# Optimization experiments

Hardware: AMD Instinct MI355X
Metric: run time of the kernel (lower is better)

The kernel has to match this reference:

```python
import jax, jax.numpy as jnp
import numpy as np

# Config from module init / global Args
H = 8        # n_head
DK = 64      # d_k
DV = 64      # d_v
D = 512      # d_model
KSZ = 3      # kernel_size (args.kernel_size)
B_PARAM = 0.001
CUR_HEAD = 3
ALPHA_C = -float(np.log(B_PARAM / (H - 1) * CUR_HEAD))  # alpha_c (nonzero head)
EPS = 1e-6


def setup_inputs() -> dict:
    key = jax.random.key(0)
    ks = jax.random.split(key, 8)
    B, L = 2, 2048
    q = jax.random.normal(ks[0], (B, L, D), jnp.float32)
    k = jax.random.normal(ks[1], (B, L, D), jnp.float32)
    v = jax.random.normal(ks[2], (B, L, D), jnp.float32)
    # Linear weights stored torch-style: [out_features, in_features]
    w_q = jax.random.normal(ks[3], (H * DK, D), jnp.float32) * 0.02
    w_k = jax.random.normal(ks[4], (H * DK, D), jnp.float32) * 0.02
    w_v = jax.random.normal(ks[5], (H * DV, D), jnp.float32) * 0.02
    w_fc = jax.random.normal(ks[6], (D, H * DV), jnp.float32) * 0.02
    gamma = jnp.ones((D,), jnp.float32)
    beta = jnp.zeros((D,), jnp.float32)
    return {"q": q, "k": k, "v": v, "w_q": w_q, "w_k": w_k, "w_v": w_v,
            "w_fc": w_fc, "gamma": gamma, "beta": beta}


def reference(q, k, v, w_q, w_k, w_v, w_fc, gamma, beta):
    B, L, _ = q.shape
    residual = q
    # QKV projections -> [B, H, L, d]
    qh = jnp.einsum('bld,ed->ble', q, w_q).reshape(B, L, H, DK).transpose(0, 2, 1, 3)
    kh = jnp.einsum('bld,ed->ble', k, w_k).reshape(B, L, H, DK).transpose(0, 2, 1, 3)
    vh = jnp.einsum('bld,ed->ble', v, w_v).reshape(B, L, H, DV).transpose(0, 2, 1, 3)
    # Scores: matmul(q / sqrt(d_k), k^T)  (LaSAttention receives d_k = d_k**0.5)
    attn = jnp.einsum('bhqd,bhkd->bhqk', qh, kh) / jnp.sqrt(jnp.float32(DK))
    # Distance weighting: eld = alpha_c * -(x - y) * attn, d_l[i,j] = j - i
    idx = jnp.arange(L)
    d_l = idx[None, :] - idx[:, None]                      # [L, L]
    eld_mat = (-ALPHA_C * d_l).astype(attn.dtype)
    eld = eld_mat[None, None, :, :] * attn
    # Softmax then avg_pool1d(kernel=KSZ, stride=1, pad=(KSZ-1)//2, count_include_pad)
    p = jax.nn.softmax(eld, axis=-1)                       # [B, H, L, L]
    pad = (KSZ - 1) // 2
    pp = jnp.pad(p, ((0, 0), (0, 0), (0, 0), (pad, pad)))
    pooled = sum(pp[..., j:j + L] for j in range(KSZ)) / jnp.float32(KSZ)
    # Value matmul (seq lengths equal so no trimming needed)
    out = jnp.einsum('bhqk,bhkd->bhqd', pooled, vh)
    out = out.transpose(0, 2, 1, 3).reshape(B, L, H * DV)
    # Output projection (dropout is identity in eval), residual, LayerNorm
    out = jnp.einsum('ble,de->bld', out, w_fc)
    out = out[:, :, None, :] + residual[:, :, None, :]     # [B, L, 1, D]
    mu = out.mean(axis=-1, keepdims=True)
    var = ((out - mu) ** 2).mean(axis=-1, keepdims=True)
    out = (out - mu) / jnp.sqrt(var + EPS) * gamma + beta
    return (out, pooled)
```

## Files before the change

kernel.cpp:

```cpp
#include <hip/hip_runtime.h>
#include <cstddef>
#include <cstdint>

#define ALPHA_C 7.7550531393693407f
constexpr int BB = 2;
constexpr int LL = 2048;
constexpr int HH = 8;
constexpr size_t OUT0  = (size_t)BB * LL * 512;
constexpr size_t PLANE = (size_t)BB * HH * LL * 64;
constexpr size_t XN    = (size_t)BB * LL * 512;
constexpr size_t WN    = (size_t)512 * 512;

typedef __attribute__((ext_vector_type(8))) short bf16x8;
typedef __attribute__((ext_vector_type(4))) short short4v;
typedef __attribute__((ext_vector_type(4))) float f32x4;

__device__ inline short f2bf(float x) {
  union { float f; unsigned u; } un; un.f = x;
  unsigned r = un.u + 0x7fffu + ((un.u >> 16) & 1u);
  return (short)(r >> 16);
}
__device__ inline float bf2f(short s) {
  union { unsigned u; float f; } un; un.u = ((unsigned)(unsigned short)s) << 16;
  return un.f;
}
__device__ inline void split3(float x, short& h, short& m, short& l) {
  h = f2bf(x); float r = x - bf2f(h);
  m = f2bf(r); float r2 = r - bf2f(m);
  l = f2bf(r2);
}

__global__ __launch_bounds__(256) void k_split3x(
    const float* __restrict__ a, const float* __restrict__ b, const float* __restrict__ c,
    short* __restrict__ da, short* __restrict__ db, short* __restrict__ dc, size_t n)
{
  size_t i = ((size_t)blockIdx.x * 256 + threadIdx.x) * 4;
  if (i >= n) return;
  const float* srcs[3] = {a, b, c};
  short* dsts[3] = {da, db, dc};
  #pragma unroll
  for (int s = 0; s < 3; ++s) {
    float4 x = *(const float4*)&srcs[s][i];
    short4v h, m, l;
    short th, tm, tl;
// ... 104 lines not shown
    for (int t = 0; t < 4; ++t) {
      const int e = n0 + t * 16 + colg, h = e >> 6, dk = e & 63;
      #pragma unroll
      for (int r = 0; r < 4; ++r) {
        const int m = m0 + w * 16 + quad * 4 + r;
        const int b = m >> 11, l = m & 2047;
        size_t base = ((size_t)(b * HH + h) * LL + l) * 64 + dk;
        short hh, mm, ll; split3(acc[t][r], hh, mm, ll);
        Y[base] = hh; Y[PLANE + base] = mm; Y[2 * PLANE + base] = ll;
      }
    }
  } else {
    const int b  = m0 >> 11;
    const int l0 = (m0 & 2047) + w * 16 + quad * 4;
    #pragma unroll
    for (int t = 0; t < 4; ++t) {
      const int e = n0 + t * 16 + colg, h = e >> 6, dk = e & 63;
      short4v s;
      #pragma unroll
      for (int r = 0; r < 4; ++r) s[r] = f2bf(acc[t][r]);
      *(short4v*)&vt[(((size_t)b * HH + h) * 64 + dk) * LL + l0] = s;
    }
  }
}

__global__ __launch_bounds__(256) void k_stats(
    const short* __restrict__ qs, const short* __restrict__ ks,
    float* __restrict__ statspart)
{
  const int i0 = blockIdx.x * 64;
  const int jh = blockIdx.y;
  const int bh = blockIdx.z;
  __shared__ short Ks[3][64 * 72];
  const int tid = threadIdx.x;
  const int lane = tid & 63, w = tid >> 6;
  const int quad = lane >> 4, colg = lane & 15, l15 = lane & 15;
  const int sr8 = tid >> 3, sc8 = (tid & 7) * 8;

  bf16x8 qf[3][2];
  {
    const size_t qoff = ((size_t)bh * LL + i0 + w * 16 + l15) * 64 + (quad << 3);
    #pragma unroll
    for (int p = 0; p < 3; ++p)
      #pragma unroll
      for (int ch = 0; ch < 2; ++ch)
        qf[p][ch] = *(const bf16x8*)&qs[p * PLANE + qoff + ch * 32];
  }

  const int jt0 = jh * 16;
  const short* kbase = ks + (size_t)bh * LL * 64;
  #pragma unroll
  for (int p = 0; p < 3; ++p)
    #pragma unroll
    for (int it = 0; it < 2; ++it) {
      int r = it * 32 + sr8;
      *(bf16x8*)&Ks[p][r * 72 + sc8] =
          *(const bf16x8*)&kbase[p * PLANE + ((size_t)jt0 * 64 + r) * 64 + sc8];
    }
  __syncthreads();

  float M[4], S[4];
  #pragma unroll
  for (int r = 0; r < 4; ++r) { M[r] = -3.0e38f; S[r] = 0.f; }

  for (int jj = 0; jj < 16; ++jj) {
    const int jt = jt0 + jj;
    const int j0 = jt * 64;
    bf16x8 kreg[3][2];
    if (jj + 1 < 16) {
      #pragma unroll
      for (int p = 0; p < 3; ++p)
        #pragma unroll
        for (int it = 0; it < 2; ++it) {
          int r = it * 32 + sr8;
          kreg[p][it] = *(const bf16x8*)&kbase[p * PLANE + ((size_t)(jt + 1) * 64 + r) * 64 + sc8];
        }
    }

    f32x4 acc[4];
    #pragma unroll
    for (int t = 0; t < 4; ++t) { acc[t][0]=0.f; acc[t][1]=0.f; acc[t][2]=0.f; acc[t][3]=0.f; }
    #pragma unroll
    for (int ch = 0; ch < 2; ++ch) {
      const int ka = (quad << 3) + ch * 32;
      #pragma unroll
      for (int t = 0; t < 4; ++t) {
        const int br = (t * 16 + l15) * 72 + ka;
        bf16x8 bh_ = *(const bf16x8*)&Ks[0][br];
        bf16x8 bm_ = *(const bf16x8*)&Ks[1][br];
        bf16x8 bl_ = *(const bf16x8*)&Ks[2][br];
        acc[t] = __builtin_amdgcn_mfma_f32_16x16x32_bf16(qf[0][ch], bh_, acc[t], 0, 0, 0);
        acc[t] = __builtin_amdgcn_mfma_f32_16x16x32_bf16(qf[0][ch], bm_, acc[t], 0, 0, 0);
        acc[t] = __builtin_amdgcn_mfma_f32_16x16x32_bf16(qf[1][ch], bh_, acc[t], 0, 0, 0);
        acc[t] = __builtin_amdgcn_mfma_f32_16x16x32_bf16(qf[0][ch], bl_, acc[t], 0, 0, 0);
        acc[t] = __builtin_amdgcn_mfma_f32_16x16x32_bf16(qf[2][ch], bh_, acc[t], 0, 0, 0);
        acc[t] = __builtin_amdgcn_mfma_f32_16x16x32_bf16(qf[1][ch], bm_, acc[t], 0, 0, 0);
      }
    }

    #pragma unroll
    for (int r = 0; r < 4; ++r) {
      const int irow = i0 + w * 16 + quad * 4 + r;
      float e0 = -ALPHA_C * (float)(j0 +  0 + colg - irow) * (acc[0][r] * 0.125f);
      float e1 = -ALPHA_C * (float)(j0 + 16 + colg - irow) * (acc[1][r] * 0.125f);
      float e2 = -ALPHA_C * (float)(j0 + 32 + colg - irow) * (acc[2][r] * 0.125f);
      float e3 = -ALPHA_C * (float)(j0 + 48 + colg - irow) * (acc[3][r] * 0.125f);
      float mx = fmaxf(fmaxf(e0, e1), fmaxf(e2, e3));
      float nM = fmaxf(M[r], mx);
      S[r] = S[r] * __expf(M[r] - nM)
           + __expf(e0 - nM) + __expf(e1 - nM) + __expf(e2 - nM) + __expf(e3 - nM);
      M[r] = nM;
    }

    __syncthreads();
    if (jj + 1 < 16) {
      #pragma unroll
      for (int p = 0; p < 3; ++p)
        #pragma unroll
        for (int it = 0; it < 2; ++it) {
          int r = it * 32 + sr8;
          *(bf16x8*)&Ks[p][r * 72 + sc8] = kreg[p][it];
        }
    }
    __syncthreads();
  }

  #pragma unroll
  for (int r = 0; r < 4; ++r) {
    float M_ = M[r], S_ = S[r];
    #pragma unroll
    for (int d = 1; d < 16; d <<= 1) {
      float Mo = __shfl_xor(M_, d);
      float So = __shfl_xor(S_, d);
      float nM = fmaxf(M_, Mo);
      S_ = S_ * __expf(M_ - nM) + So * __expf(Mo - nM);
      M_ = nM;
    }
    if (colg == 0) {
      int irow = i0 + w * 16 + quad * 4 + r;
      size_t idx = (((size_t)jh * 16 + bh) * LL + irow) * 2;
      statspart[idx] = M_; statspart[idx + 1] = S_;
    }
  }
}

__global__ __launch_bounds__(256) void k_mergestats(
    const float* __restrict__ statspart, float* __restrict__ rowstats)
{
  const size_t row = (size_t)blockIdx.x * 256 + threadIdx.x;
  float2 a = *(const float2*)&statspart[row * 2];
  float2 b = *(const float2*)&statspart[(size_t)16 * LL * 2 + row * 2];
  float nM = fmaxf(a.x, b.x);
  float S = a.y * __expf(a.x - nM) + b.y * __expf(b.x - nM);
  rowstats[row * 2] = nM; rowstats[row * 2 + 1] = S;
}

__global__ __launch_bounds__(256) void k_pool_pv(
    const short* __restrict__ qs, const short* __restrict__ ks,
    const short* __restrict__ vavgt, const float* __restrict__ rowstats,
    float* __restrict__ pooled, short* __restrict__ outh)
{
  const int i0 = blockIdx.x * 64;
  const int bh = blockIdx.y;
  const int b = bh >> 3, h = bh & 7;
  float*       Pg = pooled + (size_t)bh * LL * LL;
  const short* Vt = vavgt + (size_t)bh * 64 * LL;
  const short* kbase = ks + (size_t)bh * LL * 64;

  __shared__ short Ks[3][64 * 72];
  __shared__ short Vsm[64 * 72];
  __shared__ short Pa[2][64 * 72];
  __shared__ float Mrow[64], invSr[64], lhalo[64];

  const int tid = threadIdx.x;
  const int lane = tid & 63, w = tid >> 6;
  const int quad = lane >> 4, colg = lane & 15, l15 = lane & 15;
  const int sr8 = tid >> 3, sc8 = (tid & 7) * 8;

  bf16x8 qf[3][2];
  {
    const size_t qoff = ((size_t)bh * LL + i0 + w * 16 + l15) * 64 + (quad << 3);
    #pragma unroll
    for (int p = 0; p < 3; ++p)
      #pragma unroll
      for (int ch = 0; ch < 2; ++ch)
        qf[p][ch] = *(const bf16x8*)&qs[p * PLANE + qoff + ch * 32];
  }
  if (tid < 64) {
    float2 ms = *(const float2*)&rowstats[((size_t)bh * LL + i0 + tid) * 2];
    Mrow[tid] = ms.x; invSr[tid] = 1.0f / ms.y; lhalo[tid] = 0.f;
  }

  #pragma unroll
  for (int p = 0; p < 3; ++p)
    #pragma unroll
    for (int it = 0; it < 2; ++it) {
      int r = it * 32 + sr8;
      *(bf16x8*)&Ks[p][r * 72 + sc8] = *(const bf16x8*)&kbase[p * PLANE + (size_t)r * 64 + sc8];
    }
  __syncthreads();

  f32x4 pv[4];
  #pragma unroll
  for (int t = 0; t < 4; ++t) { pv[t][0]=0.f; pv[t][1]=0.f; pv[t][2]=0.f; pv[t][3]=0.f; }

  for (int jt = 0; jt <= 32; ++jt) {
    if (jt < 32) {
      const int j0 = jt * 64;
      f32x4 acc[4];
      #pragma unroll
      for (int t = 0; t < 4; ++t) { acc[t][0]=0.f; acc[t][1]=0.f; acc[t][2]=0.f; acc[t][3]=0.f; }
      #pragma unroll
      for (int ch = 0; ch < 2; ++ch) {
        const int ka = (quad << 3) + ch * 32;
        #pragma unroll
        for (int t = 0; t < 4; ++t) {
          const int br = (t * 16 + l15) * 72 + ka;
          bf16x8 bh_ = *(const bf16x8*)&Ks[0][br];
          bf16x8 bm_ = *(const bf16x8*)&Ks[1][br];
          bf16x8 bl_ = *(const bf16x8*)&Ks[2][br];
          acc[t] = __builtin_amdgcn_mfma_f32_16x16x32_bf16(qf[0][ch], bh_, acc[t], 0, 0, 0);
          acc[t] = __builtin_amdgcn_mfma_f32_16x16x32_bf16(qf[0][ch], bm_, acc[t], 0, 0, 0);
          acc[t] = __builtin_amdgcn_mfma_f32_16x16x32_bf16(qf[1][ch], bh_, acc[t], 0, 0, 0);
          acc[t] = __builtin_amdgcn_mfma_f32_16x16x32_bf16(qf[0][ch], bl_, acc[t], 0, 0, 0);
          acc[t] = __builtin_amdgcn_mfma_f32_16x16x32_bf16(qf[2][ch], bh_, acc[t], 0, 0, 0);
          acc[t] = __builtin_amdgcn_mfma_f32_16x16x32_bf16(qf[1][ch], bm_, acc[t], 0, 0, 0);
        }
      }
      short* Pc = Pa[jt & 1];
      #pragma unroll
      for (int r = 0; r < 4; ++r) {
        const int row = w * 16 + quad * 4 + r;
        const int irow = i0 + row;
        const float Mr = Mrow[row], iS = invSr[row];
        #pragma unroll
        for (int t = 0; t < 4; ++t) {
          int jl = t * 16 + colg;
          float e = -ALPHA_C * (float)(j0 + jl - irow) * (acc[t][r] * 0.125f);
          Pc[row * 72 + jl] = f2bf(__expf(e - Mr) * iS);
        }
      }
    }
    if (jt >= 1) {
      #pragma unroll
      for (int it = 0; it < 2; ++it) {
        int d = it * 32 + sr8;
        *(bf16x8*)&Vsm[d * 72 + sc8] = *(const bf16x8*)&Vt[(size_t)d * LL + (jt - 1) * 64 + sc8];
      }
    }
    __syncthreads();

    if (jt >= 1) {
      const short* Pp = Pa[(jt - 1) & 1];
      const short* Pn = Pa[jt & 1];
      #pragma unroll
      for (int u = 0; u < 2; ++u) {
        const int row = (u == 0) ? (tid >> 3) : (tid >> 3) + 32;
        const int c0 = (tid & 7) * 8;
        bf16x8 x = *(const bf16x8*)&Pp[row * 72 + c0];
        float xf[8];
        #pragma unroll
        for (int i = 0; i < 8; ++i) xf[i] = bf2f(x[i]);
        float lft = (c0 == 0)  ? lhalo[row] : bf2f(Pp[row * 72 + c0 - 1]);
        float rgt = (c0 == 56) ? ((jt < 32) ? bf2f(Pn[row * 72]) : 0.f)
                               : bf2f(Pp[row * 72 + c0 + 8]);
        f32x4 o0, o1;
        o0[0] = (lft   + xf[0] + xf[1]) * (1.0f/3.0f);
        o0[1] = (xf[0] + xf[1] + xf[2]) * (1.0f/3.0f);
        o0[2] = (xf[1] + xf[2] + xf[3]) * (1.0f/3.0f);
        o0[3] = (xf[2] + xf[3] + xf[4]) * (1.0f/3.0f);
        o1[0] = (xf[3] + xf[4] + xf[5]) * (1.0f/3.0f);
        o1[1] = (xf[4] + xf[5] + xf[6]) * (1.0f/3.0f);
        o1[2] = (xf[5] + xf[6] + xf[7]) * (1.0f/3.0f);
        o1[3] = (xf[6] + xf[7] + rgt  ) * (1.0f/3.0f);
        float* dst = &Pg[(size_t)(i0 + row) * LL + (jt - 1) * 64 + c0];
        __builtin_nontemporal_store(o0, (f32x4*)dst);
        __builtin_nontemporal_store(o1, (f32x4*)(dst + 4));
        if (c0 == 56) lhalo[row] = xf[7];
      }
      #pragma unroll
      for (int ch = 0; ch < 2; ++ch) {
        const int ka = (quad << 3) + ch * 32;
        bf16x8 af = *(const bf16x8*)&Pp[(w * 16 + l15) * 72 + ka];
        #pragma unroll
        for (int t = 0; t < 4; ++t) {
          bf16x8 bfv = *(const bf16x8*)&Vsm[(t * 16 + l15) * 72 + ka];
          pv[t] = __builtin_amdgcn_mfma_f32_16x16x32_bf16(af, bfv, pv[t], 0, 0, 0);
        }
      }
    }
    if (jt + 1 < 32) {
      #pragma unroll
      for (int p = 0; p < 3; ++p)
        #pragma unroll
        for (int it = 0; it < 2; ++it) {
          int r = it * 32 + sr8;
          *(bf16x8*)&Ks[p][r * 72 + sc8] =
              *(const bf16x8*)&kbase[p * PLANE + ((size_t)(jt + 1) * 64 + r) * 64 + sc8];
        }
    }
    __syncthreads();
  }

  #pragma unroll
  for (int t = 0; t < 4; ++t)
    #pragma unroll
    for (int r = 0; r < 4; ++r) {
      int i = i0 + w * 16 + quad * 4 + r;
      int d = t * 16 + colg;
      outh[((size_t)b * LL + i) * 512 + h * 64 + d] = f2bf(pv[t][r]);
    }
}

__global__ __launch_bounds__(256) void k_fc(
    const short* __restrict__ outh, const short* __restrict__ wfcb, float* __restrict__ fcout)
{
  const int n0 = blockIdx.x * 64;
  const int m0 = blockIdx.y * 64;
  __shared__ short Asm[64 * 72];
  __shared__ short Bsm[64 * 72];
  const int tid = threadIdx.x;
  const int lane = tid & 63, w = tid >> 6;
  const int sr8 = tid >> 3, sc8 = (tid & 7) * 8;

  f32x4 acc[4];
  #pragma unroll
  for (int t = 0; t < 4; ++t) { acc[t][0]=0.f; acc[t][1]=0.f; acc[t][2]=0.f; acc[t][3]=0.f; }

  for (int k0 = 0; k0 < 512; k0 += 64) {
    #pragma unroll
    for (int it = 0; it < 2; ++it) {
      int r = it * 32 + sr8;
      *(bf16x8*)&Asm[r * 72 + sc8] = *(const bf16x8*)&outh[(size_t)(m0 + r) * 512 + k0 + sc8];
      *(bf16x8*)&Bsm[r * 72 + sc8] = *(const bf16x8*)&wfcb[(size_t)(n0 + r) * 512 + k0 + sc8];
    }
    __syncthreads();
    #pragma unroll
    for (int ch = 0; ch < 2; ++ch) {
      const int ka = ((lane >> 4) << 3) + ch * 32;
      bf16x8 af = *(const bf16x8*)&Asm[(w * 16 + (lane & 15)) * 72 + ka];
      #pragma unroll
      for (int t = 0; t < 4; ++t) {
        bf16x8 bfv = *(const bf16x8*)&Bsm[(t * 16 + (lane & 15)) * 72 + ka];
        acc[t] = __builtin_amdgcn_mfma_f32_16x16x32_bf16(af, bfv, acc[t], 0, 0, 0);
// ... 44 lines not shown
}

extern "C" void kernel_launch(void* const* d_in, const int* in_sizes, int n_in,
                              void* d_out, int out_size, void* d_ws, size_t ws_size,
                              hipStream_t stream)
{
  const float* q     = (const float*)d_in[0];
  const float* k     = (const float*)d_in[1];
  const float* v     = (const float*)d_in[2];
  const float* wq    = (const float*)d_in[3];
  const float* wk    = (const float*)d_in[4];
  const float* wv    = (const float*)d_in[5];
  const float* wfc   = (const float*)d_in[6];
  const float* gamma = (const float*)d_in[7];
  const float* beta  = (const float*)d_in[8];

  float* out    = (float*)d_out;
  float* pooled = out + OUT0;

  short* xq    = (short*)d_ws;
  short* xk    = xq + 3 * XN;
  short* xv    = xk + 3 * XN;
  short* wq3   = xv + 3 * XN;
  short* wk3   = wq3 + 3 * WN;
  short* wv3   = wk3 + 3 * WN;
  short* qsp   = wv3 + 3 * WN;
  short* ksp   = qsp + 3 * PLANE;
  short* vt    = ksp + 3 * PLANE;
  short* vavgt = vt + PLANE;
  short* wfcb  = vavgt + PLANE;
  short* outh  = wfcb + WN;
  float* statspart = (float*)(outh + OUT0);
  float* rowstats  = statspart + 4 * (size_t)BB * HH * LL;
  float* fcout     = rowstats + 2 * (size_t)BB * HH * LL;

  k_split3x<<<dim3((unsigned)(XN / 4 / 256)), 256, 0, stream>>>(q, k, v, xq, xk, xv, XN);
  k_split3x<<<dim3((unsigned)(WN / 4 / 256)), 256, 0, stream>>>(wq, wk, wv, wq3, wk3, wv3, WN);
  k_cvtbf  <<<dim3((unsigned)(WN / 8 / 256)), 256, 0, stream>>>(wfc, wfcb, WN);
  k_proj   <<<dim3(24, 64), 256, 0, stream>>>(xq, xk, xv, wq3, wk3, wv3, qsp, ksp, vt);
  k_vavg   <<<dim3(1024),   256, 0, stream>>>(vt, vavgt);
  k_stats  <<<dim3(32, 2, 16), 256, 0, stream>>>(qsp, ksp, statspart);
  k_mergestats<<<dim3(128), 256, 0, stream>>>(statspart, rowstats);
  k_pool_pv<<<dim3(32, 16), 256, 0, stream>>>(qsp, ksp, vavgt, rowstats, pooled, outh);
  k_fc     <<<dim3(8, 64),  256, 0, stream>>>(outh, wfcb, fcout);
  k_ln     <<<dim3(4096),   256, 0, stream>>>(fcout, q, gamma, beta, out);
}
```

Baseline: 496.7 us.

## Tile QK score MFMAs as 2x2 warp grid to halve LDS K reads

In both the stats and pool/PV kernels, each warp now computes a 32x32 sub-tile (two row groups by two column groups) instead of a 16x64 strip. Each K fragment read from shared memory is then reused across two row groups, which halves LDS traffic for the score computation at the cost of more Q fragment registers. The stats kernel merges the two column-half partial max/sum pairs through shared memory. The pool kernel folds the softmax normalization into a single per-row log-sum constant held in registers, exp(e - (M + log S)), replacing the shared-memory max and reciprocal-sum lookup and the multiply.

```diff
diff --git a/kernel.cpp b/kernel.cpp
--- a/kernel.cpp
+++ b/kernel.cpp
@@ -180,19 +180,22 @@
   const int jh = blockIdx.y;
   const int bh = blockIdx.z;
   __shared__ short Ks[3][64 * 72];
+  __shared__ float2 MSsm[2][64];
   const int tid = threadIdx.x;
   const int lane = tid & 63, w = tid >> 6;
+  const int wr = w >> 1, wc = w & 1;
   const int quad = lane >> 4, colg = lane & 15, l15 = lane & 15;
   const int sr8 = tid >> 3, sc8 = (tid & 7) * 8;
 
-  bf16x8 qf[3][2];
-  {
-    const size_t qoff = ((size_t)bh * LL + i0 + w * 16 + l15) * 64 + (quad << 3);
+  bf16x8 qf[2][3][2];
+  #pragma unroll
+  for (int rg = 0; rg < 2; ++rg) {
+    const size_t qoff = ((size_t)bh * LL + i0 + wr * 32 + rg * 16 + l15) * 64 + (quad << 3);
     #pragma unroll
     for (int p = 0; p < 3; ++p)
       #pragma unroll
       for (int ch = 0; ch < 2; ++ch)
-        qf[p][ch] = *(const bf16x8*)&qs[p * PLANE + qoff + ch * 32];
+        qf[rg][p][ch] = *(const bf16x8*)&qs[p * PLANE + qoff + ch * 32];
   }
 
   const int jt0 = jh * 16;
@@ -207,9 +210,11 @@
     }
   __syncthreads();
 
-  float M[4], S[4];
-  #pragma unroll
-  for (int r = 0; r < 4; ++r) { M[r] = -3.0e38f; S[r] = 0.f; }
+  float M[2][4], S[2][4];
+  #pragma unroll
+  for (int rg = 0; rg < 2; ++rg)
+    #pragma unroll
+    for (int r = 0; r < 4; ++r) { M[rg][r] = -3.0e38f; S[rg][r] = 0.f; }
 
   for (int jj = 0; jj < 16; ++jj) {
     const int jt = jt0 + jj;
@@ -225,40 +230,45 @@
         }
     }
 
-    f32x4 acc[4];
-    #pragma unroll
-    for (int t = 0; t < 4; ++t) { acc[t][0]=0.f; acc[t][1]=0.f; acc[t][2]=0.f; acc[t][3]=0.f; }
+    f32x4 acc[2][2];
+    #pragma unroll
+    for (int rg = 0; rg < 2; ++rg)
+      #pragma unroll
+      for (int t = 0; t < 2; ++t) { acc[rg][t][0]=0.f; acc[rg][t][1]=0.f; acc[rg][t][2]=0.f; acc[rg][t][3]=0.f; }
     #pragma unroll
     for (int ch = 0; ch < 2; ++ch) {
       const int ka = (quad << 3) + ch * 32;
       #pragma unroll
-      for (int t = 0; t < 4; ++t) {
-        const int br = (t * 16 + l15) * 72 + ka;
+      for (int t = 0; t < 2; ++t) {
+        const int br = (wc * 32 + t * 16 + l15) * 72 + ka;
         bf16x8 bh_ = *(const bf16x8*)&Ks[0][br];
         bf16x8 bm_ = *(const bf16x8*)&Ks[1][br];
         bf16x8 bl_ = *(const bf16x8*)&Ks[2][br];
-        acc[t] = __builtin_amdgcn_mfma_f32_16x16x32_bf16(qf[0][ch], bh_, acc[t], 0, 0, 0);
-        acc[t] = __builtin_amdgcn_mfma_f32_16x16x32_bf16(qf[0][ch], bm_, acc[t], 0, 0, 0);
-        acc[t] = __builtin_amdgcn_mfma_f32_16x16x32_bf16(qf[1][ch], bh_, acc[t], 0, 0, 0);
-        acc[t] = __builtin_amdgcn_mfma_f32_16x16x32_bf16(qf[0][ch], bl_, acc[t], 0, 0, 0);
-        acc[t] = __builtin_amdgcn_mfma_f32_16x16x32_bf16(qf[2][ch], bh_, acc[t], 0, 0, 0);
-        acc[t] = __builtin_amdgcn_mfma_f32_16x16x32_bf16(qf[1][ch], bm_, acc[t], 0, 0, 0);
-      }
-    }
-
-    #pragma unroll
-    for (int r = 0; r < 4; ++r) {
-      const int irow = i0 + w * 16 + quad * 4 + r;
-      float e0 = -ALPHA_C * (float)(j0 +  0 + colg - irow) * (acc[0][r] * 0.125f);
-      float e1 = -ALPHA_C * (float)(j0 + 16 + colg - irow) * (acc[1][r] * 0.125f);
-      float e2 = -ALPHA_C * (float)(j0 + 32 + colg - irow) * (acc[2][r] * 0.125f);
-      float e3 = -ALPHA_C * (float)(j0 + 48 + colg - irow) * (acc[3][r] * 0.125f);
-      float mx = fmaxf(fmaxf(e0, e1), fmaxf(e2, e3));
-      float nM = fmaxf(M[r], mx);
-      S[r] = S[r] * __expf(M[r] - nM)
-           + __expf(e0 - nM) + __expf(e1 - nM) + __expf(e2 - nM) + __expf(e3 - nM);
-      M[r] = nM;
-    }
+        #pragma unroll
+        for (int rg = 0; rg < 2; ++rg) {
+          acc[rg][t] = __builtin_amdgcn_mfma_f32_16x16x32_bf16(qf[rg][0][ch], bh_, acc[rg][t], 0, 0, 0);
+          acc[rg][t] = __builtin_amdgcn_mfma_f32_16x16x32_bf16(qf[rg][0][ch], bm_, acc[rg][t], 0, 0, 0);
+          acc[rg][t] = __builtin_amdgcn_mfma_f32_16x16x32_bf16(qf[rg][1][ch], bh_, acc[rg][t], 0, 0, 0);
+          acc[rg][t] = __builtin_amdgcn_mfma_f32_16x16x32_bf16(qf[rg][0][ch], bl_, acc[rg][t], 0, 0, 0);
+          acc[rg][t] = __builtin_amdgcn_mfma_f32_16x16x32_bf16(qf[rg][2][ch], bh_, acc[rg][t], 0, 0, 0);
+          acc[rg][t] = __builtin_amdgcn_mfma_f32_16x16x32_bf16(qf[rg][1][ch], bm_, acc[rg][t], 0, 0, 0);
+        }
+      }
+    }
+
+    #pragma unroll
+    for (int rg = 0; rg < 2; ++rg)
+      #pragma unroll
+      for (int r = 0; r < 4; ++r) {
+        const int irow = i0 + wr * 32 + rg * 16 + quad * 4 + r;
+        float e0 = -ALPHA_C * (float)(j0 + wc * 32 +  0 + colg - irow) * (acc[rg][0][r] * 0.125f);
+        float e1 = -ALPHA_C * (float)(j0 + wc * 32 + 16 + colg - irow) * (acc[rg][1][r] * 0.125f);
+        float mx = fmaxf(e0, e1);
+        float nM = fmaxf(M[rg][r], mx);
+        S[rg][r] = S[rg][r] * __expf(M[rg][r] - nM)
+                 + __expf(e0 - nM) + __expf(e1 - nM);
+        M[rg][r] = nM;
+      }
 
     __syncthreads();
     if (jj + 1 < 16) {
@@ -274,21 +284,28 @@
   }
 
   #pragma unroll
-  for (int r = 0; r < 4; ++r) {
-    float M_ = M[r], S_ = S[r];
-    #pragma unroll
-    for (int d = 1; d < 16; d <<= 1) {
-      float Mo = __shfl_xor(M_, d);
-      float So = __shfl_xor(S_, d);
-      float nM = fmaxf(M_, Mo);
-      S_ = S_ * __expf(M_ - nM) + So * __expf(Mo - nM);
-      M_ = nM;
-    }
-    if (colg == 0) {
-      int irow = i0 + w * 16 + quad * 4 + r;
-      size_t idx = (((size_t)jh * 16 + bh) * LL + irow) * 2;
-      statspart[idx] = M_; statspart[idx + 1] = S_;
-    }
+  for (int rg = 0; rg < 2; ++rg)
+    #pragma unroll
+    for (int r = 0; r < 4; ++r) {
+      float M_ = M[rg][r], S_ = S[rg][r];
+      #pragma unroll
+      for (int d = 1; d < 16; d <<= 1) {
+        float Mo = __shfl_xor(M_, d);
+        float So = __shfl_xor(S_, d);
+        float nM = fmaxf(M_, Mo);
+        S_ = S_ * __expf(M_ - nM) + So * __expf(Mo - nM);
+        M_ = nM;
+      }
+      if (colg == 0) MSsm[wc][wr * 32 + rg * 16 + quad * 4 + r] = make_float2(M_, S_);
+    }
+  __syncthreads();
+  if (tid < 64) {
+    float2 a = MSsm[0][tid];
+    float2 b = MSsm[1][tid];
+    float nM = fmaxf(a.x, b.x);
+    float Sm = a.y * __expf(a.x - nM) + b.y * __expf(b.x - nM);
+    size_t idx = (((size_t)jh * 16 + bh) * LL + i0 + tid) * 2;
+    statspart[idx] = nM; statspart[idx + 1] = Sm;
   }
 }
 
@@ -318,26 +335,34 @@
   __shared__ short Ks[3][64 * 72];
   __shared__ short Vsm[64 * 72];
   __shared__ short Pa[2][64 * 72];
-  __shared__ float Mrow[64], invSr[64], lhalo[64];
+  __shared__ float lhalo[64];
 
   const int tid = threadIdx.x;
   const int lane = tid & 63, w = tid >> 6;
+  const int wr = w >> 1, wc = w & 1;
   const int quad = lane >> 4, colg = lane & 15, l15 = lane & 15;
   const int sr8 = tid >> 3, sc8 = (tid & 7) * 8;
 
-  bf16x8 qf[3][2];
-  {
-    const size_t qoff = ((size_t)bh * LL + i0 + w * 16 + l15) * 64 + (quad << 3);
+  bf16x8 qf[2][3][2];
+  #pragma unroll
+  for (int rg = 0; rg < 2; ++rg) {
+    const size_t qoff = ((size_t)bh * LL + i0 + wr * 32 + rg * 16 + l15) * 64 + (quad << 3);
     #pragma unroll
     for (int p = 0; p < 3; ++p)
       #pragma unroll
       for (int ch = 0; ch < 2; ++ch)
-        qf[p][ch] = *(const bf16x8*)&qs[p * PLANE + qoff + ch * 32];
-  }
-  if (tid < 64) {
-    float2 ms = *(const float2*)&rowstats[((size_t)bh * LL + i0 + tid) * 2];
-    Mrow[tid] = ms.x; invSr[tid] = 1.0f / ms.y; lhalo[tid] = 0.f;
-  }
+        qf[rg][p][ch] = *(const bf16x8*)&qs[p * PLANE + qoff + ch * 32];
+  }
+  float C[2][4];
+  #pragma unroll
+  for (int rg = 0; rg < 2; ++rg)
+    #pragma unroll
+    for (int r = 0; r < 4; ++r) {
+      const int irow = i0 + wr * 32 + rg * 16 + quad * 4 + r;
+      float2 ms = *(const float2*)&rowstats[((size_t)bh * LL + irow) * 2];
+      C[rg][r] = ms.x + __logf(ms.y);
+    }
+  if (tid < 64) lhalo[tid] = 0.f;
 
   #pragma unroll
   for (int p = 0; p < 3; ++p)
@@ -355,39 +380,45 @@
   for (int jt = 0; jt <= 32; ++jt) {
     if (jt < 32) {
       const int j0 = jt * 64;
-      f32x4 acc[4];
-      #pragma unroll
-      for (int t = 0; t < 4; ++t) { acc[t][0]=0.f; acc[t][1]=0.f; acc[t][2]=0.f; acc[t][3]=0.f; }
+      f32x4 acc[2][2];
+      #pragma unroll
+      for (int rg = 0; rg < 2; ++rg)
+        #pragma unroll
+        for (int t = 0; t < 2; ++t) { acc[rg][t][0]=0.f; acc[rg][t][1]=0.f; acc[rg][t][2]=0.f; acc[rg][t][3]=0.f; }
       #pragma unroll
       for (int ch = 0; ch < 2; ++ch) {
         const int ka = (quad << 3) + ch * 32;
         #pragma unroll
-        for (int t = 0; t < 4; ++t) {
-          const int br = (t * 16 + l15) * 72 + ka;
+        for (int t = 0; t < 2; ++t) {
+          const int br = (wc * 32 + t * 16 + l15) * 72 + ka;
           bf16x8 bh_ = *(const bf16x8*)&Ks[0][br];
           bf16x8 bm_ = *(const bf16x8*)&Ks[1][br];
           bf16x8 bl_ = *(const bf16x8*)&Ks[2][br];
-          acc[t] = __builtin_amdgcn_mfma_f32_16x16x32_bf16(qf[0][ch], bh_, acc[t], 0, 0, 0);
-          acc[t] = __builtin_amdgcn_mfma_f32_16x16x32_bf16(qf[0][ch], bm_, acc[t], 0, 0, 0);
-          acc[t] = __builtin_amdgcn_mfma_f32_16x16x32_bf16(qf[1][ch], bh_, acc[t], 0, 0, 0);
-          acc[t] = __builtin_amdgcn_mfma_f32_16x16x32_bf16(qf[0][ch], bl_, acc[t], 0, 0, 0);
-          acc[t] = __builtin_amdgcn_mfma_f32_16x16x32_bf16(qf[2][ch], bh_, acc[t], 0, 0, 0);
-          acc[t] = __builtin_amdgcn_mfma_f32_16x16x32_bf16(qf[1][ch], bm_, acc[t], 0, 0, 0);
+          #pragma unroll
+          for (int rg = 0; rg < 2; ++rg) {
+            acc[rg][t] = __builtin_amdgcn_mfma_f32_16x16x32_bf16(qf[rg][0][ch], bh_, acc[rg][t], 0, 0, 0);
+            acc[rg][t] = __builtin_amdgcn_mfma_f32_16x16x32_bf16(qf[rg][0][ch], bm_, acc[rg][t], 0, 0, 0);
+            acc[rg][t] = __builtin_amdgcn_mfma_f32_16x16x32_bf16(qf[rg][1][ch], bh_, acc[rg][t], 0, 0, 0);
+            acc[rg][t] = __builtin_amdgcn_mfma_f32_16x16x32_bf16(qf[rg][0][ch], bl_, acc[rg][t], 0, 0, 0);
+            acc[rg][t] = __builtin_amdgcn_mfma_f32_16x16x32_bf16(qf[rg][2][ch], bh_, acc[rg][t], 0, 0, 0);
+            acc[rg][t] = __builtin_amdgcn_mfma_f32_16x16x32_bf16(qf[rg][1][ch], bm_, acc[rg][t], 0, 0, 0);
+          }
         }
       }
       short* Pc = Pa[jt & 1];
       #pragma unroll
-      for (int r = 0; r < 4; ++r) {
-        const int row = w * 16 + quad * 4 + r;
-        const int irow = i0 + row;
-        const float Mr = Mrow[row], iS = invSr[row];
-        #pragma unroll
-        for (int t = 0; t < 4; ++t) {
-          int jl = t * 16 + colg;
-          float e = -ALPHA_C * (float)(j0 + jl - irow) * (acc[t][r] * 0.125f);
-          Pc[row * 72 + jl] = f2bf(__expf(e - Mr) * iS);
+      for (int rg = 0; rg < 2; ++rg)
+        #pragma unroll
+        for (int r = 0; r < 4; ++r) {
+          const int row = wr * 32 + rg * 16 + quad * 4 + r;
+          const int irow = i0 + row;
+          #pragma unroll
+          for (int t = 0; t < 2; ++t) {
+            int jl = wc * 32 + t * 16 + colg;
+            float e = -ALPHA_C * (float)(j0 + jl - irow) * (acc[rg][t][r] * 0.125f);
+            Pc[row * 72 + jl] = f2bf(__expf(e - C[rg][r]));
+          }
         }
-      }
     }
     if (jt >= 1) {
       #pragma unroll
@@ -429,7 +460,7 @@
       #pragma unroll
       for (int ch = 0; ch < 2; ++ch) {
         const int ka = (quad << 3) + ch * 32;
-        bf16x8 af = *(const bf16x8*)&Pp[(w * 16 + l15) * 72 + ka];
+        bf16x8 af = *(const bf16x8*)&Pa[(jt - 1) & 1][(w * 16 + l15) * 72 + ka];
         #pragma unroll
         for (int t = 0; t < 4; ++t) {
           bf16x8 bfv = *(const bf16x8*)&Vsm[(t * 16 + l15) * 72 + ka];
```

New measurement: 505.7 us. About the same (+1.8%).

## Split pool/PV kernel over two key halves and use exp2 softmax math

Applied to the files above, without the earlier changes.

Splits k_pool_pv along the key dimension into two z-slices, raising the grid from 512 to 1024 blocks. Each slice writes fp32 partial PV results that a new merge kernel sums and converts to bf16. The second slice recomputes one overlapping key tile so the pooling halo is correct. Softmax math moves to base-2 exponentials with precomputed distance factors and a folded log-normalizer, and the LDS row stride changes from 72 to 68. This adds a partial-buffer round trip and one more launch in exchange for better occupancy on a grid that was too small to fill the GPU.

```diff
diff --git a/kernel.cpp b/kernel.cpp
--- a/kernel.cpp
+++ b/kernel.cpp
@@ -10,6 +10,9 @@
 constexpr size_t PLANE = (size_t)BB * HH * LL * 64;
 constexpr size_t XN    = (size_t)BB * LL * 512;
 constexpr size_t WN    = (size_t)512 * 512;
+
+constexpr float AL2N   = (float)(-7.7550531393693407 * 0.125 * 1.4426950408889634);
+constexpr float AL2N16 = AL2N * 16.0f;
 
 typedef __attribute__((ext_vector_type(8))) short bf16x8;
 typedef __attribute__((ext_vector_type(4))) short short4v;
@@ -207,13 +210,14 @@
     }
   __syncthreads();
 
-  float M[4], S[4];
-  #pragma unroll
-  for (int r = 0; r < 4; ++r) { M[r] = -3.0e38f; S[r] = 0.f; }
+  float M[4], S[4], fb0[4];
+  #pragma unroll
+  for (int r = 0; r < 4; ++r) {
+    M[r] = -3.0e38f; S[r] = 0.f;
+    fb0[r] = (float)(jt0 * 64 + colg - (i0 + w * 16 + quad * 4 + r));
+  }
 
   for (int jj = 0; jj < 16; ++jj) {
-    const int jt = jt0 + jj;
-    const int j0 = jt * 64;
     bf16x8 kreg[3][2];
     if (jj + 1 < 16) {
       #pragma unroll
@@ -221,7 +225,7 @@
         #pragma unroll
         for (int it = 0; it < 2; ++it) {
           int r = it * 32 + sr8;
-          kreg[p][it] = *(const bf16x8*)&kbase[p * PLANE + ((size_t)(jt + 1) * 64 + r) * 64 + sc8];
+          kreg[p][it] = *(const bf16x8*)&kbase[p * PLANE + ((size_t)(jt0 + jj + 1) * 64 + r) * 64 + sc8];
         }
     }
 
@@ -248,16 +252,20 @@
 
     #pragma unroll
     for (int r = 0; r < 4; ++r) {
-      const int irow = i0 + w * 16 + quad * 4 + r;
-      float e0 = -ALPHA_C * (float)(j0 +  0 + colg - irow) * (acc[0][r] * 0.125f);
-      float e1 = -ALPHA_C * (float)(j0 + 16 + colg - irow) * (acc[1][r] * 0.125f);
-      float e2 = -ALPHA_C * (float)(j0 + 32 + colg - irow) * (acc[2][r] * 0.125f);
-      float e3 = -ALPHA_C * (float)(j0 + 48 + colg - irow) * (acc[3][r] * 0.125f);
+      float pe0 = AL2N * fb0[r];
+      float pe1 = pe0 + AL2N16;
+      float pe2 = pe1 + AL2N16;
+      float pe3 = pe2 + AL2N16;
+      float e0 = pe0 * acc[0][r];
+      float e1 = pe1 * acc[1][r];
+      float e2 = pe2 * acc[2][r];
+      float e3 = pe3 * acc[3][r];
       float mx = fmaxf(fmaxf(e0, e1), fmaxf(e2, e3));
       float nM = fmaxf(M[r], mx);
-      S[r] = S[r] * __expf(M[r] - nM)
-           + __expf(e0 - nM) + __expf(e1 - nM) + __expf(e2 - nM) + __expf(e3 - nM);
+      S[r] = S[r] * exp2f(M[r] - nM)
+           + exp2f(e0 - nM) + exp2f(e1 - nM) + exp2f(e2 - nM) + exp2f(e3 - nM);
       M[r] = nM;
+      fb0[r] += 64.0f;
     }
 
     __syncthreads();
@@ -281,7 +289,7 @@
       float Mo = __shfl_xor(M_, d);
       float So = __shfl_xor(S_, d);
       float nM = fmaxf(M_, Mo);
-      S_ = S_ * __expf(M_ - nM) + So * __expf(Mo - nM);
+      S_ = S_ * exp2f(M_ - nM) + So * exp2f(Mo - nM);
       M_ = nM;
     }
     if (colg == 0) {
@@ -299,26 +307,31 @@
   float2 a = *(const float2*)&statspart[row * 2];
   float2 b = *(const float2*)&statspart[(size_t)16 * LL * 2 + row * 2];
   float nM = fmaxf(a.x, b.x);
-  float S = a.y * __expf(a.x - nM) + b.y * __expf(b.x - nM);
+  float S = a.y * exp2f(a.x - nM) + b.y * exp2f(b.x - nM);
   rowstats[row * 2] = nM; rowstats[row * 2 + 1] = S;
 }
 
 __global__ __launch_bounds__(256) void k_pool_pv(
     const short* __restrict__ qs, const short* __restrict__ ks,
     const short* __restrict__ vavgt, const float* __restrict__ rowstats,
-    float* __restrict__ pooled, short* __restrict__ outh)
-{
+    float* __restrict__ pooled, float* __restrict__ pvpart)
+{
+  constexpr int LDP = 68;
   const int i0 = blockIdx.x * 64;
   const int bh = blockIdx.y;
-  const int b = bh >> 3, h = bh & 7;
+  const int jz = blockIdx.z;
+  const int jlo = jz * 16;
+  const int jstart = (jz == 0) ? 0 : 15;
+  const int qklast = (jz == 0) ? 16 : 31;
+  const int jend   = (jz == 0) ? 16 : 32;
   float*       Pg = pooled + (size_t)bh * LL * LL;
   const short* Vt = vavgt + (size_t)bh * 64 * LL;
   const short* kbase = ks + (size_t)bh * LL * 64;
 
-  __shared__ short Ks[3][64 * 72];
-  __shared__ short Vsm[64 * 72];
-  __shared__ short Pa[2][64 * 72];
-  __shared__ float Mrow[64], invSr[64], lhalo[64];
+  __shared__ short Ks[3][64 * LDP];
+  __shared__ short Vsm[64 * LDP];
+  __shared__ short Pa[2][64 * LDP];
+  __shared__ float lhalo[64];
 
   const int tid = threadIdx.x;
   const int lane = tid & 63, w = tid >> 6;
@@ -334,17 +347,23 @@
       for (int ch = 0; ch < 2; ++ch)
         qf[p][ch] = *(const bf16x8*)&qs[p * PLANE + qoff + ch * 32];
   }
-  if (tid < 64) {
-    float2 ms = *(const float2*)&rowstats[((size_t)bh * LL + i0 + tid) * 2];
-    Mrow[tid] = ms.x; invSr[tid] = 1.0f / ms.y; lhalo[tid] = 0.f;
-  }
+  float nC2[4], fb0[4];
+  #pragma unroll
+  for (int r = 0; r < 4; ++r) {
+    const int irow = i0 + w * 16 + quad * 4 + r;
+    float2 ms = *(const float2*)&rowstats[((size_t)bh * LL + irow) * 2];
+    nC2[r] = -(ms.x + log2f(ms.y));
+    fb0[r] = (float)(jstart * 64 + colg - irow);
+  }
+  if (tid < 64) lhalo[tid] = 0.f;
 
   #pragma unroll
   for (int p = 0; p < 3; ++p)
     #pragma unroll
     for (int it = 0; it < 2; ++it) {
       int r = it * 32 + sr8;
-      *(bf16x8*)&Ks[p][r * 72 + sc8] = *(const bf16x8*)&kbase[p * PLANE + (size_t)r * 64 + sc8];
+      *(bf16x8*)&Ks[p][r * LDP + sc8] =
+          *(const bf16x8*)&kbase[p * PLANE + ((size_t)jstart * 64 + r) * 64 + sc8];
     }
   __syncthreads();
 
@@ -352,9 +371,8 @@
   #pragma unroll
   for (int t = 0; t < 4; ++t) { pv[t][0]=0.f; pv[t][1]=0.f; pv[t][2]=0.f; pv[t][3]=0.f; }
 
-  for (int jt = 0; jt <= 32; ++jt) {
-    if (jt < 32) {
-      const int j0 = jt * 64;
+  for (int jt = jstart; jt <= jend; ++jt) {
+    if (jt <= qklast) {
       f32x4 acc[4];
       #pragma unroll
       for (int t = 0; t < 4; ++t) { acc[t][0]=0.f; acc[t][1]=0.f; acc[t][2]=0.f; acc[t][3]=0.f; }
@@ -363,7 +381,7 @@
         const int ka = (quad << 3) + ch * 32;
         #pragma unroll
         for (int t = 0; t < 4; ++t) {
-          const int br = (t * 16 + l15) * 72 + ka;
+          const int br = (t * 16 + l15) * LDP + ka;
           bf16x8 bh_ = *(const bf16x8*)&Ks[0][br];
           bf16x8 bm_ = *(const bf16x8*)&Ks[1][br];
           bf16x8 bl_ = *(const bf16x8*)&Ks[2][br];
@@ -379,39 +397,40 @@
       #pragma unroll
       for (int r = 0; r < 4; ++r) {
         const int row = w * 16 + quad * 4 + r;
-        const int irow = i0 + row;
-        const float Mr = Mrow[row], iS = invSr[row];
-        #pragma unroll
-        for (int t = 0; t < 4; ++t) {
-          int jl = t * 16 + colg;
-          float e = -ALPHA_C * (float)(j0 + jl - irow) * (acc[t][r] * 0.125f);
-          Pc[row * 72 + jl] = f2bf(__expf(e - Mr) * iS);
-        }
-      }
-    }
-    if (jt >= 1) {
+        float pe0 = AL2N * fb0[r];
+        float pe1 = pe0 + AL2N16;
+        float pe2 = pe1 + AL2N16;
+        float pe3 = pe2 + AL2N16;
+        Pc[row * LDP +      colg] = f2bf(exp2f(fmaf(pe0, acc[0][r], nC2[r])));
+        Pc[row * LDP + 16 + colg] = f2bf(exp2f(fmaf(pe1, acc[1][r], nC2[r])));
+        Pc[row * LDP + 32 + colg] = f2bf(exp2f(fmaf(pe2, acc[2][r], nC2[r])));
+        Pc[row * LDP + 48 + colg] = f2bf(exp2f(fmaf(pe3, acc[3][r], nC2[r])));
+        fb0[r] += 64.0f;
+      }
+    }
+    if (jt > jlo) {
       #pragma unroll
       for (int it = 0; it < 2; ++it) {
         int d = it * 32 + sr8;
-        *(bf16x8*)&Vsm[d * 72 + sc8] = *(const bf16x8*)&Vt[(size_t)d * LL + (jt - 1) * 64 + sc8];
-      }
-    }
-    __syncthreads();
-
-    if (jt >= 1) {
+        *(bf16x8*)&Vsm[d * LDP + sc8] = *(const bf16x8*)&Vt[(size_t)d * LL + (jt - 1) * 64 + sc8];
+      }
+    }
+    __syncthreads();
+
+    if (jt > jlo) {
       const short* Pp = Pa[(jt - 1) & 1];
       const short* Pn = Pa[jt & 1];
       #pragma unroll
       for (int u = 0; u < 2; ++u) {
         const int row = (u == 0) ? (tid >> 3) : (tid >> 3) + 32;
         const int c0 = (tid & 7) * 8;
-        bf16x8 x = *(const bf16x8*)&Pp[row * 72 + c0];
+        bf16x8 x = *(const bf16x8*)&Pp[row * LDP + c0];
         float xf[8];
         #pragma unroll
         for (int i = 0; i < 8; ++i) xf[i] = bf2f(x[i]);
-        float lft = (c0 == 0)  ? lhalo[row] : bf2f(Pp[row * 72 + c0 - 1]);
-        float rgt = (c0 == 56) ? ((jt < 32) ? bf2f(Pn[row * 72]) : 0.f)
-                               : bf2f(Pp[row * 72 + c0 + 8]);
+        float lft = (c0 == 0)  ? lhalo[row] : bf2f(Pp[row * LDP + c0 - 1]);
+        float rgt = (c0 == 56) ? ((jt <= qklast) ? bf2f(Pn[row * LDP]) : 0.f)
+                               : bf2f(Pp[row * LDP + c0 + 8]);
         f32x4 o0, o1;
         o0[0] = (lft   + xf[0] + xf[1]) * (1.0f/3.0f);
         o0[1] = (xf[0] + xf[1] + xf[2]) * (1.0f/3.0f);
@@ -429,21 +448,28 @@
       #pragma unroll
       for (int ch = 0; ch < 2; ++ch) {
         const int ka = (quad << 3) + ch * 32;
-        bf16x8 af = *(const bf16x8*)&Pp[(w * 16 + l15) * 72 + ka];
+        bf16x8 af = *(const bf16x8*)&Pp[(w * 16 + l15) * LDP + ka];
         #pragma unroll
         for (int t = 0; t < 4; ++t) {
-          bf16x8 bfv = *(const bf16x8*)&Vsm[(t * 16 + l15) * 72 + ka];
+          bf16x8 bfv = *(const bf16x8*)&Vsm[(t * 16 + l15) * LDP + ka];
           pv[t] = __builtin_amdgcn_mfma_f32_16x16x32_bf16(af, bfv, pv[t], 0, 0, 0);
         }
       }
-    }
-    if (jt + 1 < 32) {
+    } else if (jz == 1 && jt == jlo) {
+      if ((tid & 7) == 7) {
+        const short* Pp = Pa[(jt - 1) & 1];
+        const int row = tid >> 3;
+        lhalo[row]      = bf2f(Pp[row * LDP + 63]);
+        lhalo[row + 32] = bf2f(Pp[(row + 32) * LDP + 63]);
+      }
+    }
+    if (jt + 1 <= qklast) {
       #pragma unroll
       for (int p = 0; p < 3; ++p)
         #pragma unroll
         for (int it = 0; it < 2; ++it) {
           int r = it * 32 + sr8;
-          *(bf16x8*)&Ks[p][r * 72 + sc8] =
+          *(bf16x8*)&Ks[p][r * LDP + sc8] =
               *(const bf16x8*)&kbase[p * PLANE + ((size_t)(jt + 1) * 64 + r) * 64 + sc8];
         }
     }
@@ -456,8 +482,24 @@
     for (int r = 0; r < 4; ++r) {
       int i = i0 + w * 16 + quad * 4 + r;
       int d = t * 16 + colg;
-      outh[((size_t)b * LL + i) * 512 + h * 64 + d] = f2bf(pv[t][r]);
-    }
+      pvpart[(((size_t)(jz * 16 + bh)) * LL + i) * 64 + d] = pv[t][r];
+    }
+}
+
+__global__ __launch_bounds__(256) void k_pvmerge(
+    const float* __restrict__ pvpart, short* __restrict__ outh)
+{
+  const size_t idx = ((size_t)blockIdx.x * 256 + threadIdx.x) * 4;
+  f32x4 a = *(const f32x4*)&pvpart[idx];
+  f32x4 b = *(const f32x4*)&pvpart[(size_t)16 * LL * 64 + idx];
+  const int bh = (int)(idx >> 17);
+  const int rem = (int)(idx & 131071);
+  const int i = rem >> 6, d = rem & 63;
+  const int bb = bh >> 3, h = bh & 7;
+  short4v o;
+  #pragma unroll
+  for (int t = 0; t < 4; ++t) o[t] = f2bf(a[t] + b[t]);
+  *(short4v*)&outh[((size_t)bb * LL + i) * 512 + h * 64 + d] = o;
 }
 
 __global__ __launch_bounds__(256) void k_fc(
@@ -568,7 +610,8 @@
   short* outh  = wfcb + WN;
   float* statspart = (float*)(outh + OUT0);
   float* rowstats  = statspart + 4 * (size_t)BB * HH * LL;
-  float* fcout     = rowstats + 2 * (size_t)BB * HH * LL;
+  float* pvpart    = rowstats + 2 * (size_t)BB * HH * LL;
+  float* fcout     = pvpart + (size_t)2 * 16 * LL * 64;
 
   k_split3x<<<dim3((unsigned)(XN / 4 / 256)), 256, 0, stream>>>(q, k, v, xq, xk, xv, XN);
   k_split3x<<<dim3((unsigned)(WN / 4 / 256)), 256, 0, stream>>>(wq, wk, wv, wq3, wk3, wv3, WN);
@@ -577,7 +620,8 @@
   k_vavg   <<<dim3(1024),   256, 0, stream>>>(vt, vavgt);
   k_stats  <<<dim3(32, 2, 16), 256, 0, stream>>>(qsp, ksp, statspart);
   k_mergestats<<<dim3(128), 256, 0, stream>>>(statspart, rowstats);
-  k_pool_pv<<<dim3(32, 16), 256, 0, stream>>>(qsp, ksp, vavgt, rowstats, pooled, outh);
+  k_pool_pv<<<dim3(32, 16, 2), 256, 0, stream>>>(qsp, ksp, vavgt, rowstats, pooled, pvpart);
+  k_pvmerge<<<dim3(2048),   256, 0, stream>>>(pvpart, outh);
   k_fc     <<<dim3(8, 64),  256, 0, stream>>>(outh, wfcb, fcout);
   k_ln     <<<dim3(4096),   256, 0, stream>>>(fcout, q, gamma, beta, out);
 }
```

Measured after the change: 528.5 us. 6.4% more time.

## Halve pool_pv row tile, split warps over columns, use exp2 with folded constants

Applied to the files above, without the earlier changes.

The softmax exponent now runs in base 2 with the alpha, scale and log2e constants folded together. The distance factor is computed incrementally, and row normalisation is folded into a single fma before exp2 in both the stats and pool kernels. k_pool_pv now processes 32 rows per block instead of 64, doubling the grid. Its four waves are split 2x2 over rows and columns, and V tiles are loaded straight from global into registers instead of being staged in shared memory. The aim is higher occupancy and less ALU, LDS and barrier work on the dominant pool/PV kernel, at the cost of reloading each K tile twice as often overall.

```diff
diff --git a/kernel.cpp b/kernel.cpp
--- a/kernel.cpp
+++ b/kernel.cpp
@@ -10,6 +10,9 @@
 constexpr size_t PLANE = (size_t)BB * HH * LL * 64;
 constexpr size_t XN    = (size_t)BB * LL * 512;
 constexpr size_t WN    = (size_t)512 * 512;
+
+constexpr float AL2N   = (float)(-7.7550531393693407 * 0.125 * 1.4426950408889634);
+constexpr float AL2N16 = AL2N * 16.0f;
 
 typedef __attribute__((ext_vector_type(8))) short bf16x8;
 typedef __attribute__((ext_vector_type(4))) short short4v;
@@ -207,13 +210,14 @@
     }
   __syncthreads();
 
-  float M[4], S[4];
-  #pragma unroll
-  for (int r = 0; r < 4; ++r) { M[r] = -3.0e38f; S[r] = 0.f; }
+  float M[4], S[4], fb0[4];
+  #pragma unroll
+  for (int r = 0; r < 4; ++r) {
+    M[r] = -3.0e38f; S[r] = 0.f;
+    fb0[r] = (float)(jt0 * 64 + colg - (i0 + w * 16 + quad * 4 + r));
+  }
 
   for (int jj = 0; jj < 16; ++jj) {
-    const int jt = jt0 + jj;
-    const int j0 = jt * 64;
     bf16x8 kreg[3][2];
     if (jj + 1 < 16) {
       #pragma unroll
@@ -221,7 +225,7 @@
         #pragma unroll
         for (int it = 0; it < 2; ++it) {
           int r = it * 32 + sr8;
-          kreg[p][it] = *(const bf16x8*)&kbase[p * PLANE + ((size_t)(jt + 1) * 64 + r) * 64 + sc8];
+          kreg[p][it] = *(const bf16x8*)&kbase[p * PLANE + ((size_t)(jt0 + jj + 1) * 64 + r) * 64 + sc8];
         }
     }
 
@@ -248,16 +252,20 @@
 
     #pragma unroll
     for (int r = 0; r < 4; ++r) {
-      const int irow = i0 + w * 16 + quad * 4 + r;
-      float e0 = -ALPHA_C * (float)(j0 +  0 + colg - irow) * (acc[0][r] * 0.125f);
-      float e1 = -ALPHA_C * (float)(j0 + 16 + colg - irow) * (acc[1][r] * 0.125f);
-      float e2 = -ALPHA_C * (float)(j0 + 32 + colg - irow) * (acc[2][r] * 0.125f);
-      float e3 = -ALPHA_C * (float)(j0 + 48 + colg - irow) * (acc[3][r] * 0.125f);
+      float pe0 = AL2N * fb0[r];
+      float pe1 = pe0 + AL2N16;
+      float pe2 = pe1 + AL2N16;
+      float pe3 = pe2 + AL2N16;
+      float e0 = pe0 * acc[0][r];
+      float e1 = pe1 * acc[1][r];
+      float e2 = pe2 * acc[2][r];
+      float e3 = pe3 * acc[3][r];
       float mx = fmaxf(fmaxf(e0, e1), fmaxf(e2, e3));
       float nM = fmaxf(M[r], mx);
-      S[r] = S[r] * __expf(M[r] - nM)
-           + __expf(e0 - nM) + __expf(e1 - nM) + __expf(e2 - nM) + __expf(e3 - nM);
+      S[r] = S[r] * exp2f(M[r] - nM)
+           + exp2f(e0 - nM) + exp2f(e1 - nM) + exp2f(e2 - nM) + exp2f(e3 - nM);
       M[r] = nM;
+      fb0[r] += 64.0f;
     }
 
     __syncthreads();
@@ -281,7 +289,7 @@
       float Mo = __shfl_xor(M_, d);
       float So = __shfl_xor(S_, d);
       float nM = fmaxf(M_, Mo);
-      S_ = S_ * __expf(M_ - nM) + So * __expf(Mo - nM);
+      S_ = S_ * exp2f(M_ - nM) + So * exp2f(Mo - nM);
       M_ = nM;
     }
     if (colg == 0) {
@@ -299,7 +307,7 @@
   float2 a = *(const float2*)&statspart[row * 2];
   float2 b = *(const float2*)&statspart[(size_t)16 * LL * 2 + row * 2];
   float nM = fmaxf(a.x, b.x);
-  float S = a.y * __expf(a.x - nM) + b.y * __expf(b.x - nM);
+  float S = a.y * exp2f(a.x - nM) + b.y * exp2f(b.x - nM);
   rowstats[row * 2] = nM; rowstats[row * 2 + 1] = S;
 }
 
@@ -308,7 +316,7 @@
     const short* __restrict__ vavgt, const float* __restrict__ rowstats,
     float* __restrict__ pooled, short* __restrict__ outh)
 {
-  const int i0 = blockIdx.x * 64;
+  const int i0 = blockIdx.x * 32;
   const int bh = blockIdx.y;
   const int b = bh >> 3, h = bh & 7;
   float*       Pg = pooled + (size_t)bh * LL * LL;
@@ -316,28 +324,33 @@
   const short* kbase = ks + (size_t)bh * LL * 64;
 
   __shared__ short Ks[3][64 * 72];
-  __shared__ short Vsm[64 * 72];
-  __shared__ short Pa[2][64 * 72];
-  __shared__ float Mrow[64], invSr[64], lhalo[64];
+  __shared__ short Pa[2][32 * 72];
+  __shared__ float lhalo[32];
 
   const int tid = threadIdx.x;
   const int lane = tid & 63, w = tid >> 6;
+  const int wr = w >> 1, wc = w & 1;
   const int quad = lane >> 4, colg = lane & 15, l15 = lane & 15;
   const int sr8 = tid >> 3, sc8 = (tid & 7) * 8;
 
   bf16x8 qf[3][2];
   {
-    const size_t qoff = ((size_t)bh * LL + i0 + w * 16 + l15) * 64 + (quad << 3);
+    const size_t qoff = ((size_t)bh * LL + i0 + wr * 16 + l15) * 64 + (quad << 3);
     #pragma unroll
     for (int p = 0; p < 3; ++p)
       #pragma unroll
       for (int ch = 0; ch < 2; ++ch)
         qf[p][ch] = *(const bf16x8*)&qs[p * PLANE + qoff + ch * 32];
   }
-  if (tid < 64) {
-    float2 ms = *(const float2*)&rowstats[((size_t)bh * LL + i0 + tid) * 2];
-    Mrow[tid] = ms.x; invSr[tid] = 1.0f / ms.y; lhalo[tid] = 0.f;
-  }
+  float nC2[4], fb0[4];
+  #pragma unroll
+  for (int r = 0; r < 4; ++r) {
+    const int irow = i0 + wr * 16 + quad * 4 + r;
+    float2 ms = *(const float2*)&rowstats[((size_t)bh * LL + irow) * 2];
+    nC2[r] = -(ms.x + log2f(ms.y));
+    fb0[r] = (float)(wc * 32 + colg - irow);
+  }
+  if (tid < 32) lhalo[tid] = 0.f;
 
   #pragma unroll
   for (int p = 0; p < 3; ++p)
@@ -348,22 +361,30 @@
     }
   __syncthreads();
 
-  f32x4 pv[4];
-  #pragma unroll
-  for (int t = 0; t < 4; ++t) { pv[t][0]=0.f; pv[t][1]=0.f; pv[t][2]=0.f; pv[t][3]=0.f; }
+  f32x4 pv[2];
+  #pragma unroll
+  for (int t = 0; t < 2; ++t) { pv[t][0]=0.f; pv[t][1]=0.f; pv[t][2]=0.f; pv[t][3]=0.f; }
+  bf16x8 vreg[2][2];
 
   for (int jt = 0; jt <= 32; ++jt) {
+    if (jt >= 1) {
+      #pragma unroll
+      for (int t = 0; t < 2; ++t)
+        #pragma unroll
+        for (int ch = 0; ch < 2; ++ch)
+          vreg[t][ch] = *(const bf16x8*)&Vt[(size_t)(wc * 32 + t * 16 + l15) * LL
+                                            + (jt - 1) * 64 + (quad << 3) + ch * 32];
+    }
     if (jt < 32) {
-      const int j0 = jt * 64;
-      f32x4 acc[4];
-      #pragma unroll
-      for (int t = 0; t < 4; ++t) { acc[t][0]=0.f; acc[t][1]=0.f; acc[t][2]=0.f; acc[t][3]=0.f; }
+      f32x4 acc[2];
+      #pragma unroll
+      for (int t = 0; t < 2; ++t) { acc[t][0]=0.f; acc[t][1]=0.f; acc[t][2]=0.f; acc[t][3]=0.f; }
       #pragma unroll
       for (int ch = 0; ch < 2; ++ch) {
         const int ka = (quad << 3) + ch * 32;
         #pragma unroll
-        for (int t = 0; t < 4; ++t) {
-          const int br = (t * 16 + l15) * 72 + ka;
+        for (int t = 0; t < 2; ++t) {
+          const int br = (wc * 32 + t * 16 + l15) * 72 + ka;
           bf16x8 bh_ = *(const bf16x8*)&Ks[0][br];
           bf16x8 bm_ = *(const bf16x8*)&Ks[1][br];
           bf16x8 bl_ = *(const bf16x8*)&Ks[2][br];
@@ -378,22 +399,12 @@
       short* Pc = Pa[jt & 1];
       #pragma unroll
       for (int r = 0; r < 4; ++r) {
-        const int row = w * 16 + quad * 4 + r;
-        const int irow = i0 + row;
-        const float Mr = Mrow[row], iS = invSr[row];
-        #pragma unroll
-        for (int t = 0; t < 4; ++t) {
-          int jl = t * 16 + colg;
-          float e = -ALPHA_C * (float)(j0 + jl - irow) * (acc[t][r] * 0.125f);
-          Pc[row * 72 + jl] = f2bf(__expf(e - Mr) * iS);
-        }
-      }
-    }
-    if (jt >= 1) {
-      #pragma unroll
-      for (int it = 0; it < 2; ++it) {
-        int d = it * 32 + sr8;
-        *(bf16x8*)&Vsm[d * 72 + sc8] = *(const bf16x8*)&Vt[(size_t)d * LL + (jt - 1) * 64 + sc8];
+        const int row = wr * 16 + quad * 4 + r;
+        float pe0 = AL2N * fb0[r];
+        float pe1 = pe0 + AL2N16;
+        Pc[row * 72 + wc * 32 +      colg] = f2bf(exp2f(fmaf(pe0, acc[0][r], nC2[r])));
+        Pc[row * 72 + wc * 32 + 16 + colg] = f2bf(exp2f(fmaf(pe1, acc[1][r], nC2[r])));
+        fb0[r] += 64.0f;
       }
     }
     __syncthreads();
@@ -401,9 +412,8 @@
     if (jt >= 1) {
       const short* Pp = Pa[(jt - 1) & 1];
       const short* Pn = Pa[jt & 1];
-      #pragma unroll
-      for (int u = 0; u < 2; ++u) {
-        const int row = (u == 0) ? (tid >> 3) : (tid >> 3) + 32;
+      {
+        const int row = tid >> 3;
         const int c0 = (tid & 7) * 8;
         bf16x8 x = *(const bf16x8*)&Pp[row * 72 + c0];
         float xf[8];
@@ -429,12 +439,10 @@
       #pragma unroll
       for (int ch = 0; ch < 2; ++ch) {
         const int ka = (quad << 3) + ch * 32;
-        bf16x8 af = *(const bf16x8*)&Pp[(w * 16 + l15) * 72 + ka];
-        #pragma unroll
-        for (int t = 0; t < 4; ++t) {
-          bf16x8 bfv = *(const bf16x8*)&Vsm[(t * 16 + l15) * 72 + ka];
-          pv[t] = __builtin_amdgcn_mfma_f32_16x16x32_bf16(af, bfv, pv[t], 0, 0, 0);
-        }
+        bf16x8 af = *(const bf16x8*)&Pp[(wr * 16 + l15) * 72 + ka];
+        #pragma unroll
+        for (int t = 0; t < 2; ++t)
+          pv[t] = __builtin_amdgcn_mfma_f32_16x16x32_bf16(af, vreg[t][ch], pv[t], 0, 0, 0);
       }
     }
     if (jt + 1 < 32) {
@@ -451,11 +459,11 @@
   }
 
   #pragma unroll
-  for (int t = 0; t < 4; ++t)
+  for (int t = 0; t < 2; ++t)
     #pragma unroll
     for (int r = 0; r < 4; ++r) {
-      int i = i0 + w * 16 + quad * 4 + r;
-      int d = t * 16 + colg;
+      int i = i0 + wr * 16 + quad * 4 + r;
+      int d = wc * 32 + t * 16 + colg;
       outh[((size_t)b * LL + i) * 512 + h * 64 + d] = f2bf(pv[t][r]);
     }
 }
@@ -577,7 +585,7 @@
   k_vavg   <<<dim3(1024),   256, 0, stream>>>(vt, vavgt);
   k_stats  <<<dim3(32, 2, 16), 256, 0, stream>>>(qsp, ksp, statspart);
   k_mergestats<<<dim3(128), 256, 0, stream>>>(statspart, rowstats);
-  k_pool_pv<<<dim3(32, 16), 256, 0, stream>>>(qsp, ksp, vavgt, rowstats, pooled, outh);
+  k_pool_pv<<<dim3(64, 16), 256, 0, stream>>>(qsp, ksp, vavgt, rowstats, pooled, outh);
   k_fc     <<<dim3(8, 64),  256, 0, stream>>>(outh, wfcb, fcout);
   k_ln     <<<dim3(4096),   256, 0, stream>>>(fcout, q, gamma, beta, out);
 }
```

After: 550.1 us. +10.8%, slower.
